# Kernel optimization log

Hardware: AMD Instinct MI355X
Metric: run time of the kernel (lower is better)

The kernel has to match this reference:

```python
import jax, jax.numpy as jnp
import numpy as np

B, TT, C, H, T = 4, 4096, 1024, 16, 128
K = C // H  # head size (rk and v head sizes equal here)
HEAD_DIV = 8.0  # head_size_divisor
EPS = 1e-5  # GroupNorm eps
LAYER_ID, N_LAYER = 12, 24


def setup_inputs() -> dict:
    key = jax.random.key(0)
    ks = jax.random.split(key, 8)
    r01 = LAYER_ID / (N_LAYER - 1)
    r1a0 = 1.0 - LAYER_ID / N_LAYER
    ddd = (jnp.arange(C, dtype=jnp.float32) / C).reshape(1, 1, C)
    h = jnp.arange(H, dtype=jnp.float32)
    scale = 0.02
    return {
        "xq": jax.random.normal(ks[0], (B, TT, C), jnp.float32),
        "time_mix_k": ddd ** r1a0,
        "time_mix_v": ddd ** r1a0 + 0.3 * r01,
        "time_mix_r": ddd ** (0.5 * r1a0),
        "time_mix_g": ddd ** (0.5 * r1a0),
        "time_decay": -8.0 + 7.0 * (h / (H - 1)) ** (0.7 + 1.3 * r01),
        "time_faaaa": r01 * (1.0 - h / (H - 1)),
        "W_r": jax.random.normal(ks[1], (C, C), jnp.float32) * scale,
        "W_k": jax.random.normal(ks[2], (C, C), jnp.float32) * scale,
        "W_v": jax.random.normal(ks[3], (C, C), jnp.float32) * scale,
        "W_g": jax.random.normal(ks[4], (C, C), jnp.float32) * scale,
        "W_o": jax.random.normal(ks[5], (C, C), jnp.float32) * scale,
        "ln_w": jnp.ones((C,), jnp.float32),
        "ln_b": jnp.zeros((C,), jnp.float32),
    }


def reference(xq, time_mix_k, time_mix_v, time_mix_r, time_mix_g,
              time_decay, time_faaaa, W_r, W_k, W_v, W_g, W_o, ln_w, ln_b):
    x = xq
    B_, TT_, C_ = x.shape
    N = TT_ // T  # number of chunks
    # time shift: xx[:, t] = x[:, t-1], xx[:, 0] = 0
    xx = jnp.pad(x, ((0, 0), (1, 0), (0, 0)))[:, :-1]
    xr = x * time_mix_r + xx * (1 - time_mix_r)
    xk = x * time_mix_k + xx * (1 - time_mix_k)
    xv = x * time_mix_v + xx * (1 - time_mix_v)
    xg = x * time_mix_g + xx * (1 - time_mix_g)
    r = (xr @ W_r.T).reshape(B_, TT_, H, K).transpose(0, 2, 1, 3)  # (B,H,TT,K)
    k = (xk @ W_k.T).reshape(B_, TT_, H, K).transpose(0, 2, 1, 3)
    v = (xv @ W_v.T).reshape(B_, TT_, H, K).transpose(0, 2, 1, 3)
    g = jax.nn.silu(xg @ W_g.T)  # (B,TT,C)

    decay = jnp.exp(-jnp.exp(time_decay))  # (H,)
    u = time_faaaa  # (H,)
    ws = decay ** T  # per-chunk state decay (H,)
    i_idx = jnp.arange(T)
    wb = decay[:, None] ** i_idx                # (H,T): decay^i
    wk = decay[:, None] ** (T - 1 - i_idx)      # (H,T): decay^(T-1-j)
    diff = i_idx[:, None] - i_idx[None, :]      # i - j
    pw = decay[:, None, None] ** jnp.maximum(diff - 1, 0)
    # lower-triangular intra-chunk decay: decay^(i-j-1) for i>j, u on diag
    w_mat = jnp.where(diff > 0, pw, 0.0) + jnp.eye(T, dtype=x.dtype) * u[:, None, None]  # (H,T,T)

    # chunked layout: (N, B, H, T, K)
    rc = r.reshape(B_, H, N, T, K).transpose(2, 0, 1, 3, 4)
    kc = k.reshape(B_, H, N, T, K).transpose(2, 0, 1, 3, 4)
    vc = v.reshape(B_, H, N, T, K).transpose(2, 0, 1, 3, 4)
    s0 = jnp.zeros((B_, H, K, K), x.dtype)

    def step(s, chunk):
        rr, kk, vv = chunk
        att = jnp.einsum('bhik,bhjk->bhij', rr, kk) * w_mat
        out = att @ vv + jnp.einsum('bhik,bhkv->bhiv', rr, s) * wb[None, :, :, None]
        s_new = ws[None, :, None, None] * s + jnp.einsum(
            'bhjk,bhjv->bhkv', kk * wk[None, :, :, None], vv)
        return s_new, out

    _, xo = jax.lax.scan(step, s0, (rc, kc, vc))  # xo: (N,B,H,T,K)
    xo = xo.transpose(1, 0, 3, 2, 4).reshape(B_, TT_, H, K)

    # GroupNorm(H groups) over channels, applied to x / head_size_divisor
    y = xo / HEAD_DIV
    mu = y.mean(-1, keepdims=True)
    var = y.var(-1, keepdims=True)
    y = (y - mu) / jnp.sqrt(var + EPS)
    y = y * ln_w.reshape(H, K) + ln_b.reshape(H, K)
    y = y.reshape(B_, TT_, C_)
    return (y * g) @ W_o.T
```

## Files before the change

### kernel.cpp

```cpp
#include <hip/hip_runtime.h>
#include <hip/hip_bf16.h>
#include <stdint.h>

#define C_DIM 1024
#define H_DIM 16
#define K_DIM 64
#define T_CH 128
#define TT_DIM 4096
#define B_DIM 4
#define N_CH 32
#define M_ROWS 16384

typedef __attribute__((ext_vector_type(8))) __bf16 bf16x8;
typedef __attribute__((ext_vector_type(4))) float floatx4;

__device__ __forceinline__ float bf2f(ushort u) {
  union { uint32_t i; float f; } v; v.i = ((uint32_t)u) << 16; return v.f;
}
__device__ __forceinline__ ushort f2bf(float f) {
  union { float f; uint32_t i; } v; v.f = f;
  return (ushort)((v.i + 0x7fffu + ((v.i >> 16) & 1u)) >> 16);
}

#define GLOAD_LDS16(g, l)                                                     \
  __builtin_amdgcn_global_load_lds(                                           \
      (const __attribute__((address_space(1))) void*)(g),                     \
      (__attribute__((address_space(3))) void*)(l), 16, 0, 0)

__global__ __launch_bounds__(256) void mix_kernel(
    const float* __restrict__ x,
    const float* __restrict__ mk, const float* __restrict__ mv,
    const float* __restrict__ mr, const float* __restrict__ mg,
    ushort* __restrict__ xr, ushort* __restrict__ xk,
    ushort* __restrict__ xv, ushort* __restrict__ xg) {
  long idx = (long)blockIdx.x * 256 + threadIdx.x;
  long e = idx * 8;
  int c = (int)(e & (C_DIM - 1));
  long row = e >> 10;
  int t = (int)(row & (TT_DIM - 1));
  floatx4 xc0 = *(const floatx4*)(x + e);
  floatx4 xc1 = *(const floatx4*)(x + e + 4);
  floatx4 xp0 = {0.f, 0.f, 0.f, 0.f};
  floatx4 xp1 = {0.f, 0.f, 0.f, 0.f};
  if (t != 0) {
    xp0 = *(const floatx4*)(x + e - C_DIM);
    xp1 = *(const floatx4*)(x + e - C_DIM + 4);
  }
  floatx4 d0 = xc0 - xp0;
  floatx4 d1 = xc1 - xp1;
  union { ushort u[8]; uint4 q; } pk;
#define ST(dst, mptr)                                                         \
  {                                                                           \
    floatx4 m0 = *(const floatx4*)((mptr) + c);                               \
    floatx4 m1 = *(const floatx4*)((mptr) + c + 4);                           \
    floatx4 o0 = xp0 + d0 * m0;                                               \
    floatx4 o1 = xp1 + d1 * m1;                                               \
    pk.u[0] = f2bf(o0.x); pk.u[1] = f2bf(o0.y);                               \
    pk.u[2] = f2bf(o0.z); pk.u[3] = f2bf(o0.w);                               \
    pk.u[4] = f2bf(o1.x); pk.u[5] = f2bf(o1.y);                               \
    pk.u[6] = f2bf(o1.z); pk.u[7] = f2bf(o1.w);                               \
    *(uint4*)((dst) + e) = pk.q;                                              \
  }
  ST(xk, mk) ST(xv, mv) ST(xr, mr) ST(xg, mg)
#undef ST
}

__global__ __launch_bounds__(256) void wconv_kernel(
    const float* __restrict__ w0, const float* __restrict__ w1,
    const float* __restrict__ w2, const float* __restrict__ w3,
    const float* __restrict__ w4, ushort* __restrict__ o) {
  long idx = (long)blockIdx.x * 256 + threadIdx.x;
  long e = idx * 8;
  int wi = (int)(e >> 20);
  long off = e & ((1L << 20) - 1);
  const float* src = wi == 0 ? w0 : wi == 1 ? w1 : wi == 2 ? w2 : wi == 3 ? w3 : w4;
  floatx4 v0 = *(const floatx4*)(src + off);
  floatx4 v1 = *(const floatx4*)(src + off + 4);
  union { ushort u[8]; uint4 q; } pk;
  pk.u[0] = f2bf(v0.x); pk.u[1] = f2bf(v0.y);
  pk.u[2] = f2bf(v0.z); pk.u[3] = f2bf(v0.w);
  pk.u[4] = f2bf(v1.x); pk.u[5] = f2bf(v1.y);
  pk.u[6] = f2bf(v1.z); pk.u[7] = f2bf(v1.w);
  *(uint4*)(o + e) = pk.q;
}

#define BARX() __builtin_amdgcn_s_barrier()
#define SCHEDB() __builtin_amdgcn_sched_barrier(0)
#define VMW4() asm volatile("s_waitcnt vmcnt(4)" ::: "memory")
#define VMW0() asm volatile("s_waitcnt vmcnt(0)" ::: "memory")
#define LGKW() asm volatile("s_waitcnt lgkmcnt(0)" ::: "memory")

template <int EPI>
__global__ __launch_bounds__(512, 2) void gemm_bt(
    const ushort* __restrict__ A, const ushort* __restrict__ Bt,
    void* __restrict__ Cout) {
  __shared__ __align__(16) ushort smem[65536];
  const int tid = threadIdx.x;
  const int lane = tid & 63, w = tid >> 6;
  const int q = lane >> 4, l16 = lane & 15;
  const int wm = w >> 2, wn = w & 3;
  const int id = blockIdx.x;
  const int wg = (id & 7) * 32 + (id >> 3);
  const int bm = wg >> 2, bn = wg & 3;

  const int r8 = tid >> 3;
  const int c8 = ((tid & 7) ^ (r8 & 7)) * 8;
  const ushort* gA = A + (long)(bm * 256 + r8) * C_DIM + c8;
  const ushort* gB = Bt + (long)(bn * 256 + r8) * C_DIM + c8;

  const char* sB = (const char*)smem;
  const int arow = (wm * 128 + l16) * 128;
  const int brow = (wn * 64 + l16) * 128;
  const int swz = (l16 & 7) << 4;
  const int csv[2] = {(q << 4) ^ swz, ((4 + q) << 4) ^ swz};

  floatx4 acc[8][4] = {};
  bf16x8 af[4][2];
  bf16x8 bfv[4][2];

#define STAGE(ISA, sl, hh, tile)                                              \
  do {                                                                        \
    const ushort* g_ = (ISA ? gA : gB) + ((hh) * 131072 + (tile) * 64);       \
    ushort* l_ = smem + ((ISA ? 0 : 32768) + (sl) * 16384 + (hh) * 8192 +     \
                         w * 512);                                            \
    GLOAD_LDS16(g_, l_);                                                      \
    GLOAD_LDS16(g_ + 65536, l_ + 4096);                                       \
  } while (0)

#define READ_A(sl, qr)                                                        \
  do {                                                                        \
    _Pragma("unroll") for (int i_ = 0; i_ < 4; ++i_) {                        \
      af[i_][0] = *(const bf16x8*)(sB + (sl) * 32768 + arow + (qr) * 8192 +   \
                                   i_ * 2048 + csv[0]);                       \
      af[i_][1] = *(const bf16x8*)(sB + (sl) * 32768 + arow + (qr) * 8192 +   \
                                   i_ * 2048 + csv[1]);                       \
    }                                                                         \
  } while (0)

#define READ_B(sl, qc)                                                        \
  do {                                                                        \
    _Pragma("unroll") for (int j_ = 0; j_ < 2; ++j_) {                        \
      bfv[(qc) * 2 + j_][0] = *(const bf16x8*)(sB + 65536 + (sl) * 32768 +    \
                                               brow + (qc) * 4096 +           \
                                               j_ * 2048 + csv[0]);           \
      bfv[(qc) * 2 + j_][1] = *(const bf16x8*)(sB + 65536 + (sl) * 32768 +    \
                                               brow + (qc) * 4096 +           \
                                               j_ * 2048 + csv[1]);           \
    }                                                                         \
  } while (0)

#define MFMA_Q(qr, qc)                                                        \
  do {                                                                        \
    __builtin_amdgcn_s_setprio(1);                                            \
    _Pragma("unroll") for (int i_ = 0; i_ < 4; ++i_)                          \
        _Pragma("unroll") for (int j_ = 0; j_ < 2; ++j_) {                    \
      acc[(qr) * 4 + i_][(qc) * 2 + j_] =                                     \
          __builtin_amdgcn_mfma_f32_16x16x32_bf16(                            \
              af[i_][0], bfv[(qc) * 2 + j_][0],                               \
              acc[(qr) * 4 + i_][(qc) * 2 + j_], 0, 0, 0);                    \
      acc[(qr) * 4 + i_][(qc) * 2 + j_] =                                     \
          __builtin_amdgcn_mfma_f32_16x16x32_bf16(                            \
              af[i_][1], bfv[(qc) * 2 + j_][1],                               \
              acc[(qr) * 4 + i_][(qc) * 2 + j_], 0, 0, 0);                    \
    }                                                                         \
    __builtin_amdgcn_s_setprio(0);                                            \
  } while (0)

  STAGE(1, 0, 0, 0); STAGE(1, 0, 1, 0);
  STAGE(0, 0, 0, 0); STAGE(0, 0, 1, 0);
  STAGE(0, 1, 0, 1); STAGE(0, 1, 1, 1);
  VMW4();
  BARX();
  SCHEDB();
  READ_B(0, 0);

#pragma unroll 1
  for (int i = 0; i < 7; ++i) {
    const int t1 = 2 * i + 1, tn0 = 2 * i + 2, tn1 = 2 * i + 3;
    READ_A(0, 0); STAGE(1, 1, 0, t1);
    BARX(); SCHEDB(); READ_B(0, 1); MFMA_Q(0, 0); LGKW(); BARX();
    STAGE(1, 1, 1, t1);
    BARX(); SCHEDB(); MFMA_Q(0, 1); LGKW(); BARX();
    READ_A(0, 1); STAGE(0, 0, 0, tn0);
    BARX(); SCHEDB(); MFMA_Q(1, 0); LGKW(); BARX();
    STAGE(0, 0, 1, tn0); VMW4();
    BARX(); SCHEDB(); READ_B(1, 0); MFMA_Q(1, 1); LGKW(); BARX();
    READ_A(1, 0); STAGE(1, 0, 0, tn0);
    BARX(); SCHEDB(); READ_B(1, 1); MFMA_Q(0, 0); LGKW(); BARX();
    STAGE(1, 0, 1, tn0);
    BARX(); SCHEDB(); MFMA_Q(0, 1); LGKW(); BARX();
    READ_A(1, 1); STAGE(0, 1, 0, tn1);
    BARX(); SCHEDB(); MFMA_Q(1, 0); LGKW(); BARX();
    STAGE(0, 1, 1, tn1); VMW4();
    BARX(); SCHEDB(); READ_B(0, 0); MFMA_Q(1, 1); LGKW(); BARX();
  }
  READ_A(0, 0); STAGE(1, 1, 0, 15);
  BARX(); SCHEDB(); READ_B(0, 1); MFMA_Q(0, 0); LGKW(); BARX();
  STAGE(1, 1, 1, 15);
  BARX(); SCHEDB(); MFMA_Q(0, 1); LGKW(); BARX();
  READ_A(0, 1);
  BARX(); SCHEDB(); MFMA_Q(1, 0); LGKW(); BARX();
  VMW0();
  BARX(); SCHEDB(); READ_B(1, 0); MFMA_Q(1, 1); LGKW(); BARX();
  READ_A(1, 0);
  BARX(); SCHEDB(); READ_B(1, 1); MFMA_Q(0, 0); LGKW(); BARX();
  BARX(); SCHEDB(); MFMA_Q(0, 1); LGKW(); BARX();
  READ_A(1, 1);
  BARX(); SCHEDB(); MFMA_Q(1, 0); LGKW(); BARX();
  BARX(); MFMA_Q(1, 1);

  const int row0 = bm * 256 + wm * 128 + q * 4;
  const int col0 = bn * 256 + wn * 64 + l16;
#pragma unroll
  for (int fi = 0; fi < 8; ++fi)
#pragma unroll
    for (int fj = 0; fj < 4; ++fj)
#pragma unroll
      for (int rg = 0; rg < 4; ++rg) {
        long off = (long)(row0 + fi * 16 + rg) * C_DIM + col0 + fj * 16;
        float val = acc[fi][fj][rg];
        if (EPI == 1) val = val / (1.f + expf(-val));
        if (EPI == 2)
          ((float*)Cout)[off] = val;
        else
          ((ushort*)Cout)[off] = f2bf(val);
      }
#undef STAGE
#undef READ_A
#undef READ_B
#undef MFMA_Q
}

__global__ __launch_bounds__(256) void chunk_state(
    const ushort* __restrict__ kB, const ushort* __restrict__ vB,
    const float* __restrict__ td, ushort* __restrict__ Zc) {
  __shared__ __align__(16) ushort vt_s[64 * 136];
  __shared__ __align__(16) ushort kwt_s[64 * 136];
  int blk = blockIdx.x;
  int bh = blk >> 5, n = blk & 31;
  int b = bh >> 4, h = bh & 15;
  int tid = threadIdx.x;
  int lane = tid & 63, w = tid >> 6;
  int q = lane >> 4, l16 = lane & 15;
  float etd = expf(td[h]);
  long cbase = ((long)b * TT_DIM + n * T_CH) * C_DIM + h * K_DIM;

#pragma unroll
  for (int it = 0; it < 4; it++) {
    int chunk = it * 256 + tid;
    int row = chunk >> 3;
    int cc = (chunk & 7) * 8;
    long ga = cbase + (long)row * C_DIM + cc;
    uint4 kv4 = *(const uint4*)(kB + ga);
    uint4 vv4 = *(const uint4*)(vB + ga);
    float wkj = expf(-(float)(T_CH - 1 - row) * etd);
    const ushort* kp = (const ushort*)&kv4;
    const ushort* vp = (const ushort*)&vv4;
    int cb2 = row >> 3;
#pragma unroll
    for (int e2 = 0; e2 < 8; e2++) {
      int vr = cc + e2;
      int ph = vr * 136 + ((cb2 ^ ((vr >> 3) & 7)) << 3) + (row & 7);
      kwt_s[ph] = f2bf(bf2f(kp[e2]) * wkj);
      vt_s[ph] = vp[e2];
    }
  }
  __syncthreads();

  floatx4 accZ[4] = {};
#pragma unroll
  for (int js = 0; js < 128; js += 32) {
    int cb = q + (js >> 3);
    int vrA = w * 16 + l16;
    bf16x8 av = *(const bf16x8*)&vt_s[vrA * 136 + ((cb ^ ((vrA >> 3) & 7)) << 3)];
    bf16x8 bk3[4];
#pragma unroll
    for (int kt = 0; kt < 4; kt++) {
      int vrB = kt * 16 + l16;
      bk3[kt] = *(const bf16x8*)&kwt_s[vrB * 136 + ((cb ^ ((vrB >> 3) & 7)) << 3)];
    }
#pragma unroll
    for (int kt = 0; kt < 4; kt++)
      accZ[kt] = __builtin_amdgcn_mfma_f32_16x16x32_bf16(av, bk3[kt], accZ[kt], 0, 0, 0);
  }
  long zbase = (long)blk * 4096;
#pragma unroll
  for (int kt = 0; kt < 4; kt++)
#pragma unroll
    for (int rg = 0; rg < 4; rg++)
      Zc[zbase + (w * 16 + q * 4 + rg) * 64 + kt * 16 + l16] = f2bf(accZ[kt][rg]);
}

__global__ __launch_bounds__(256) void state_scan(
    const ushort* __restrict__ Zc, const float* __restrict__ td,
    ushort* __restrict__ Sb) {
  long tg = (long)blockIdx.x * 256 + threadIdx.x;
  int bh = (int)(tg >> 12);
  int e = (int)(tg & 4095);
  int h = bh & 15;
  float wsf = expf(-128.f * expf(td[h]));
  float s = 0.f;
  long base = (long)bh * N_CH * 4096 + e;
#pragma unroll
  for (int n = 0; n < N_CH; n++) {
    Sb[base + n * 4096] = f2bf(s);
    s = wsf * s + bf2f(Zc[base + n * 4096]);
  }
}

__global__ __launch_bounds__(512, 4) void chunk_out(
    const ushort* __restrict__ rB, const ushort* __restrict__ kB,
    const ushort* __restrict__ vB, const ushort* __restrict__ gBuf,
    const ushort* __restrict__ Sb,
    const float* __restrict__ td, const float* __restrict__ tf,
    const float* __restrict__ lnw, const float* __restrict__ lnb,
    ushort* __restrict__ gy) {
  __shared__ __align__(16) ushort rr_s[128 * 72];
  __shared__ __align__(16) ushort un_s[128 * 136];
  __shared__ __align__(16) ushort vt_s[64 * 136];
  __shared__ __align__(16) ushort z_s[64 * 72];
  __shared__ float pw_s[128];

  int blk = blockIdx.x;
  int bh = blk >> 5, n = blk & 31;
  int b = bh >> 4, h = bh & 15;
  int tid = threadIdx.x;
  int lane = tid & 63, w = tid >> 6;
  int q = lane >> 4, l16 = lane & 15;

  float etd = expf(td[h]);
  float u = tf[h];
  long cbase = ((long)b * TT_DIM + n * T_CH) * C_DIM + h * K_DIM;

  if (tid < 128) pw_s[tid] = expf(-(float)tid * etd);

#pragma unroll
  for (int it = 0; it < 2; it++) {
    int chunk = it * 512 + tid;
    int row = chunk >> 3;
    int cc = (chunk & 7) * 8;
    long ga = cbase + (long)row * C_DIM + cc;
    *(uint4*)&rr_s[row * 72 + cc] = *(const uint4*)(rB + ga);
    *(uint4*)&un_s[row * 136 + cc] = *(const uint4*)(kB + ga);
    uint4 vv4 = *(const uint4*)(vB + ga);
    const ushort* vp = (const ushort*)&vv4;
    int cb2 = row >> 3;
#pragma unroll
    for (int e2 = 0; e2 < 8; e2++) {
      int vr = cc + e2;
      vt_s[vr * 136 + ((cb2 ^ ((vr >> 3) & 7)) << 3) + (row & 7)] = vp[e2];
    }
  }
  {
    long sbase = (long)blk * 4096;
    int v = tid >> 3, c0 = (tid & 7) * 8;
    *(uint4*)&z_s[v * 72 + c0] = *(const uint4*)(Sb + sbase + v * 64 + c0);
  }
  __syncthreads();

  int ar0 = (w >> 1) * 32, ac0 = (w & 1) * 64;
  floatx4 accA[2][4] = {};
#pragma unroll
  for (int ks = 0; ks < 64; ks += 32) {
    bf16x8 af[2], bk2[4];
#pragma unroll
    for (int i = 0; i < 2; i++)
      af[i] = *(const bf16x8*)&rr_s[(ar0 + i * 16 + l16) * 72 + q * 8 + ks];
#pragma unroll
    for (int j = 0; j < 4; j++)
      bk2[j] = *(const bf16x8*)&un_s[(ac0 + j * 16 + l16) * 136 + q * 8 + ks];
#pragma unroll
    for (int mi = 0; mi < 2; mi++)
#pragma unroll
      for (int nj = 0; nj < 4; nj++)
        accA[mi][nj] = __builtin_amdgcn_mfma_f32_16x16x32_bf16(
            af[mi], bk2[nj], accA[mi][nj], 0, 0, 0);
  }

  int i0 = w * 16;
  floatx4 accB[4] = {};
#pragma unroll
  for (int ks = 0; ks < 64; ks += 32) {
    bf16x8 af2 = *(const bf16x8*)&rr_s[(i0 + l16) * 72 + q * 8 + ks];
    bf16x8 bz[4];
#pragma unroll
    for (int vt2 = 0; vt2 < 4; vt2++)
      bz[vt2] = *(const bf16x8*)&z_s[(vt2 * 16 + l16) * 72 + q * 8 + ks];
#pragma unroll
    for (int vt2 = 0; vt2 < 4; vt2++)
      accB[vt2] = __builtin_amdgcn_mfma_f32_16x16x32_bf16(
          af2, bz[vt2], accB[vt2], 0, 0, 0);
  }
  __syncthreads();

#pragma unroll
  for (int mi = 0; mi < 2; mi++)
#pragma unroll
    for (int nj = 0; nj < 4; nj++)
#pragma unroll
      for (int rg = 0; rg < 4; rg++) {
        int i = ar0 + mi * 16 + q * 4 + rg;
        int j = ac0 + nj * 16 + l16;
        float wv = 0.f;
        if (i > j) wv = pw_s[i - j - 1];
        else if (i == j) wv = u;
        un_s[i * 136 + j] = f2bf(accA[mi][nj][rg] * wv);
      }
  __syncthreads();

  floatx4 accO[4] = {};
#pragma unroll
  for (int js = 0; js < 128; js += 32) {
    bf16x8 af3 = *(const bf16x8*)&un_s[(i0 + l16) * 136 + q * 8 + js];
    int cb = q + (js >> 3);
    bf16x8 bv[4];
#pragma unroll
    for (int vt2 = 0; vt2 < 4; vt2++) {
      int vr = vt2 * 16 + l16;
      bv[vt2] = *(const bf16x8*)&vt_s[vr * 136 + ((cb ^ ((vr >> 3) & 7)) << 3)];
    }
#pragma unroll
    for (int vt2 = 0; vt2 < 4; vt2++)
      accO[vt2] = __builtin_amdgcn_mfma_f32_16x16x32_bf16(
          af3, bv[vt2], accO[vt2], 0, 0, 0);
  }

#pragma unroll
  for (int rg = 0; rg < 4; rg++) {
    int i = i0 + q * 4 + rg;
    float wbi = pw_s[i];
    float vals[4];
    float s1 = 0.f, s2 = 0.f;
#pragma unroll
    for (int vt2 = 0; vt2 < 4; vt2++) {
      float val = accO[vt2][rg] + wbi * accB[vt2][rg];
      vals[vt2] = val; s1 += val; s2 += val * val;
    }
#pragma unroll
    for (int mm = 1; mm < 16; mm <<= 1) {
      s1 += __shfl_xor(s1, mm, 64);
      s2 += __shfl_xor(s2, mm, 64);
    }
    float mu = s1 * (1.f / 64.f);
    float va = s2 * (1.f / 64.f) - mu * mu;
    float rinv = rsqrtf(va + 64.f * 1e-5f);
    long rowg = (long)b * TT_DIM + n * T_CH + i;
#pragma unroll
    for (int vt2 = 0; vt2 < 4; vt2++) {
      int c = h * K_DIM + vt2 * 16 + l16;
      float y = (vals[vt2] - mu) * rinv * lnw[c] + lnb[c];
      float gf = bf2f(gBuf[rowg * C_DIM + c]);
      gy[rowg * C_DIM + c] = f2bf(y * gf);
    }
  }
}

extern "C" void kernel_launch(void* const* d_in, const int* in_sizes, int n_in,
                              void* d_out, int out_size, void* d_ws,
                              size_t ws_size, hipStream_t stream) {
  const float* xq  = (const float*)d_in[0];
  const float* tmk = (const float*)d_in[1];
  const float* tmv = (const float*)d_in[2];
  const float* tmr = (const float*)d_in[3];
  const float* tmg = (const float*)d_in[4];
  const float* td  = (const float*)d_in[5];
  const float* tf  = (const float*)d_in[6];
  const float* Wr  = (const float*)d_in[7];
  const float* Wk  = (const float*)d_in[8];
  const float* Wv  = (const float*)d_in[9];
  const float* Wg  = (const float*)d_in[10];
  const float* Wo  = (const float*)d_in[11];
  const float* lnw = (const float*)d_in[12];
  const float* lnb = (const float*)d_in[13];

  char* ws = (char*)d_ws;
  const size_t BUF = (size_t)M_ROWS * C_DIM * 2;
  ushort* b0 = (ushort*)(ws + 0 * BUF);
  ushort* b1 = (ushort*)(ws + 1 * BUF);
  ushort* b2 = (ushort*)(ws + 2 * BUF);
  ushort* b3 = (ushort*)(ws + 3 * BUF);
  ushort* wcv = (ushort*)(ws + 4 * BUF);
  const ushort* wr_b = wcv;
  const ushort* wk_b = wcv + (1 << 20);
  const ushort* wv_b = wcv + 2 * (1 << 20);
  const ushort* wg_b = wcv + 3 * (1 << 20);
  const ushort* wo_b = wcv + 4 * (1 << 20);
  ushort* Zc = (ushort*)(ws + 4 * BUF + 5 * (2 << 20));
  ushort* Sb = Zc + (size_t)64 * N_CH * 4096;
  ushort* rbuf = (ushort*)d_out;

  mix_kernel<<<8192, 256, 0, stream>>>(xq, tmk, tmv, tmr, tmg, b0, b1, b2, b3);
  wconv_kernel<<<2560, 256, 0, stream>>>(Wr, Wk, Wv, Wg, Wo, wcv);

  gemm_bt<0><<<256, 512, 0, stream>>>(b0, wr_b, rbuf);
  gemm_bt<0><<<256, 512, 0, stream>>>(b1, wk_b, b0);
  gemm_bt<0><<<256, 512, 0, stream>>>(b2, wv_b, b1);
  gemm_bt<1><<<256, 512, 0, stream>>>(b3, wg_b, b2);

  chunk_state<<<2048, 256, 0, stream>>>(b0, b1, td, Zc);
  state_scan<<<1024, 256, 0, stream>>>(Zc, td, Sb);
  chunk_out<<<2048, 512, 0, stream>>>(rbuf, b0, b1, b2, Sb, td, tf, lnw, lnb, b3);

  gemm_bt<2><<<256, 512, 0, stream>>>(b3, wo_b, (float*)d_out);
}
```

Before: 405.8 us.

## Fuse time-shift mixing into projection GEMM A-operand loading

Removes the standalone mix kernel and adds a gemm_mix kernel. It loads fp32 x and the shifted previous row, applies the per-channel mix coefficient, converts to bf16 and writes the A tile into LDS inside the GEMM pipeline. This avoids writing four bf16 mixed activation buffers to memory and reading them back. In exchange each of the four GEMMs reads fp32 x twice (current and previous row), roughly four times the A-operand bytes of before. It also adds VALU conversion work and register pressure inside the MFMA loop.

```diff
diff --git a/kernel.cpp b/kernel.cpp
--- a/kernel.cpp
+++ b/kernel.cpp
@@ -26,44 +26,6 @@
   __builtin_amdgcn_global_load_lds(                                           \
       (const __attribute__((address_space(1))) void*)(g),                     \
       (__attribute__((address_space(3))) void*)(l), 16, 0, 0)
-
-__global__ __launch_bounds__(256) void mix_kernel(
-    const float* __restrict__ x,
-    const float* __restrict__ mk, const float* __restrict__ mv,
-    const float* __restrict__ mr, const float* __restrict__ mg,
-    ushort* __restrict__ xr, ushort* __restrict__ xk,
-    ushort* __restrict__ xv, ushort* __restrict__ xg) {
-  long idx = (long)blockIdx.x * 256 + threadIdx.x;
-  long e = idx * 8;
-  int c = (int)(e & (C_DIM - 1));
-  long row = e >> 10;
-  int t = (int)(row & (TT_DIM - 1));
-  floatx4 xc0 = *(const floatx4*)(x + e);
-  floatx4 xc1 = *(const floatx4*)(x + e + 4);
-  floatx4 xp0 = {0.f, 0.f, 0.f, 0.f};
-  floatx4 xp1 = {0.f, 0.f, 0.f, 0.f};
-  if (t != 0) {
-    xp0 = *(const floatx4*)(x + e - C_DIM);
-    xp1 = *(const floatx4*)(x + e - C_DIM + 4);
-  }
-  floatx4 d0 = xc0 - xp0;
-  floatx4 d1 = xc1 - xp1;
-  union { ushort u[8]; uint4 q; } pk;
-#define ST(dst, mptr)                                                         \
-  {                                                                           \
-    floatx4 m0 = *(const floatx4*)((mptr) + c);                               \
-    floatx4 m1 = *(const floatx4*)((mptr) + c + 4);                           \
-    floatx4 o0 = xp0 + d0 * m0;                                               \
-    floatx4 o1 = xp1 + d1 * m1;                                               \
-    pk.u[0] = f2bf(o0.x); pk.u[1] = f2bf(o0.y);                               \
-    pk.u[2] = f2bf(o0.z); pk.u[3] = f2bf(o0.w);                               \
-    pk.u[4] = f2bf(o1.x); pk.u[5] = f2bf(o1.y);                               \
-    pk.u[6] = f2bf(o1.z); pk.u[7] = f2bf(o1.w);                               \
-    *(uint4*)((dst) + e) = pk.q;                                              \
-  }
-  ST(xk, mk) ST(xv, mv) ST(xr, mr) ST(xg, mg)
-#undef ST
-}
 
 __global__ __launch_bounds__(256) void wconv_kernel(
     const float* __restrict__ w0, const float* __restrict__ w1,
@@ -87,8 +49,200 @@
 #define BARX() __builtin_amdgcn_s_barrier()
 #define SCHEDB() __builtin_amdgcn_sched_barrier(0)
 #define VMW4() asm volatile("s_waitcnt vmcnt(4)" ::: "memory")
+#define VMW22() asm volatile("s_waitcnt vmcnt(22)" ::: "memory")
 #define VMW0() asm volatile("s_waitcnt vmcnt(0)" ::: "memory")
 #define LGKW() asm volatile("s_waitcnt lgkmcnt(0)" ::: "memory")
+
+template <int EPI>
+__global__ __launch_bounds__(512, 2) void gemm_mix(
+    const float* __restrict__ X, const float* __restrict__ coef,
+    const ushort* __restrict__ Bt, void* __restrict__ Cout) {
+  __shared__ __align__(16) ushort smem[65536];
+  const int tid = threadIdx.x;
+  const int lane = tid & 63, w = tid >> 6;
+  const int q = lane >> 4, l16 = lane & 15;
+  const int wm = w >> 2, wn = w & 3;
+  const int id = blockIdx.x;
+  const int wg = (id & 7) * 32 + (id >> 3);
+  const int bm = wg >> 2, bn = wg & 3;
+
+  const int r8 = tid >> 3;
+  const int c8 = ((tid & 7) ^ (r8 & 7)) * 8;
+  const int arowg = bm * 256 + r8;
+  const float* Xb = X + (long)arowg * C_DIM + c8;
+  const float* Cfb = coef + c8;
+  const ushort* gB = Bt + (long)(bn * 256 + r8) * C_DIM + c8;
+
+  const char* sB = (const char*)smem;
+  const int arow = (wm * 128 + l16) * 128;
+  const int brow = (wn * 64 + l16) * 128;
+  const int swz = (l16 & 7) << 4;
+  const int csv[2] = {(q << 4) ^ swz, ((4 + q) << 4) ^ swz};
+
+  floatx4 acc[8][4] = {};
+  bf16x8 af[4][2];
+  bf16x8 bfv[4][2];
+  floatx4 mxc[4], mxp[4], mcf[2];
+
+#define STAGE_B(sl, hh, tile)                                                 \
+  do {                                                                        \
+    const ushort* g_ = gB + ((hh) * 131072 + (tile) * 64);                    \
+    ushort* l_ = smem + (32768 + (sl) * 16384 + (hh) * 8192 + w * 512);       \
+    GLOAD_LDS16(g_, l_);                                                      \
+    GLOAD_LDS16(g_ + 65536, l_ + 4096);                                       \
+  } while (0)
+
+#define MISSUE(tile, hh, WCF)                                                 \
+  do {                                                                        \
+    const float* p0_ = Xb + ((long)((hh) * 128) << 10) + (tile) * 64;         \
+    const float* p1_ = p0_ + (64 << 10);                                      \
+    mxc[0] = *(const floatx4*)p0_;                                            \
+    mxc[1] = *(const floatx4*)(p0_ + 4);                                      \
+    mxc[2] = *(const floatx4*)p1_;                                            \
+    mxc[3] = *(const floatx4*)(p1_ + 4);                                      \
+    floatx4 z_ = {0.f, 0.f, 0.f, 0.f};                                        \
+    if (((arowg + (hh) * 128) & (TT_DIM - 1)) != 0) {                         \
+      mxp[0] = *(const floatx4*)(p0_ - C_DIM);                                \
+      mxp[1] = *(const floatx4*)(p0_ - C_DIM + 4);                            \
+    } else { mxp[0] = z_; mxp[1] = z_; }                                      \
+    if (((arowg + (hh) * 128 + 64) & (TT_DIM - 1)) != 0) {                    \
+      mxp[2] = *(const floatx4*)(p1_ - C_DIM);                                \
+      mxp[3] = *(const floatx4*)(p1_ - C_DIM + 4);                            \
+    } else { mxp[2] = z_; mxp[3] = z_; }                                      \
+    if (WCF) {                                                                \
+      mcf[0] = *(const floatx4*)(Cfb + (tile) * 64);                          \
+      mcf[1] = *(const floatx4*)(Cfb + (tile) * 64 + 4);                      \
+    }                                                                         \
+  } while (0)
+
+#define MWRITE(sl, hh)                                                        \
+  do {                                                                        \
+    union { ushort u[8]; uint4 qq; } pk_;                                     \
+    floatx4 d0_ = mxc[0] - mxp[0];                                            \
+    floatx4 o0_ = mxp[0] + d0_ * mcf[0];                                      \
+    floatx4 d1_ = mxc[1] - mxp[1];                                            \
+    floatx4 o1_ = mxp[1] + d1_ * mcf[1];                                      \
+    pk_.u[0] = f2bf(o0_.x); pk_.u[1] = f2bf(o0_.y);                           \
+    pk_.u[2] = f2bf(o0_.z); pk_.u[3] = f2bf(o0_.w);                           \
+    pk_.u[4] = f2bf(o1_.x); pk_.u[5] = f2bf(o1_.y);                           \
+    pk_.u[6] = f2bf(o1_.z); pk_.u[7] = f2bf(o1_.w);                           \
+    *(uint4*)(smem + ((sl) * 16384 + (hh) * 8192 + tid * 8)) = pk_.qq;        \
+    floatx4 d2_ = mxc[2] - mxp[2];                                            \
+    floatx4 o2_ = mxp[2] + d2_ * mcf[0];                                      \
+    floatx4 d3_ = mxc[3] - mxp[3];                                            \
+    floatx4 o3_ = mxp[3] + d3_ * mcf[1];                                      \
+    pk_.u[0] = f2bf(o2_.x); pk_.u[1] = f2bf(o2_.y);                           \
+    pk_.u[2] = f2bf(o2_.z); pk_.u[3] = f2bf(o2_.w);                           \
+    pk_.u[4] = f2bf(o3_.x); pk_.u[5] = f2bf(o3_.y);                           \
+    pk_.u[6] = f2bf(o3_.z); pk_.u[7] = f2bf(o3_.w);                           \
+    *(uint4*)(smem + ((sl) * 16384 + (hh) * 8192 + 4096 + tid * 8)) = pk_.qq; \
+  } while (0)
+
+#define READ_A(sl, qr)                                                        \
+  do {                                                                        \
+    _Pragma("unroll") for (int i_ = 0; i_ < 4; ++i_) {                        \
+      af[i_][0] = *(const bf16x8*)(sB + (sl) * 32768 + arow + (qr) * 8192 +   \
+                                   i_ * 2048 + csv[0]);                       \
+      af[i_][1] = *(const bf16x8*)(sB + (sl) * 32768 + arow + (qr) * 8192 +   \
+                                   i_ * 2048 + csv[1]);                       \
+    }                                                                         \
+  } while (0)
+
+#define READ_B(sl, qc)                                                        \
+  do {                                                                        \
+    _Pragma("unroll") for (int j_ = 0; j_ < 2; ++j_) {                        \
+      bfv[(qc) * 2 + j_][0] = *(const bf16x8*)(sB + 65536 + (sl) * 32768 +    \
+                                               brow + (qc) * 4096 +           \
+                                               j_ * 2048 + csv[0]);           \
+      bfv[(qc) * 2 + j_][1] = *(const bf16x8*)(sB + 65536 + (sl) * 32768 +    \
+                                               brow + (qc) * 4096 +           \
+                                               j_ * 2048 + csv[1]);           \
+    }                                                                         \
+  } while (0)
+
+#define MFMA_Q(qr, qc)                                                        \
+  do {                                                                        \
+    __builtin_amdgcn_s_setprio(1);                                            \
+    _Pragma("unroll") for (int i_ = 0; i_ < 4; ++i_)                          \
+        _Pragma("unroll") for (int j_ = 0; j_ < 2; ++j_) {                    \
+      acc[(qr) * 4 + i_][(qc) * 2 + j_] =                                     \
+          __builtin_amdgcn_mfma_f32_16x16x32_bf16(                            \
+              af[i_][0], bfv[(qc) * 2 + j_][0],                               \
+              acc[(qr) * 4 + i_][(qc) * 2 + j_], 0, 0, 0);                    \
+      acc[(qr) * 4 + i_][(qc) * 2 + j_] =                                     \
+          __builtin_amdgcn_mfma_f32_16x16x32_bf16(                            \
+              af[i_][1], bfv[(qc) * 2 + j_][1],                               \
+              acc[(qr) * 4 + i_][(qc) * 2 + j_], 0, 0, 0);                    \
+    }                                                                         \
+    __builtin_amdgcn_s_setprio(0);                                            \
+  } while (0)
+
+  MISSUE(0, 0, 1); MWRITE(0, 0);
+  MISSUE(0, 1, 0); MWRITE(0, 1);
+  STAGE_B(0, 0, 0); STAGE_B(0, 1, 0);
+  STAGE_B(1, 0, 1); STAGE_B(1, 1, 1);
+  MISSUE(1, 0, 1);
+  VMW4();
+  LGKW();
+  BARX();
+  SCHEDB();
+  READ_B(0, 0);
+
+#pragma unroll 1
+  for (int i = 0; i < 7; ++i) {
+    const int t1 = 2 * i + 1, tn0 = 2 * i + 2, tn1 = 2 * i + 3;
+    READ_A(0, 0); MWRITE(1, 0); MISSUE(t1, 1, 0);
+    BARX(); SCHEDB(); READ_B(0, 1); MFMA_Q(0, 0); LGKW(); BARX();
+    MWRITE(1, 1);
+    BARX(); SCHEDB(); MFMA_Q(0, 1); LGKW(); BARX();
+    READ_A(0, 1); STAGE_B(0, 0, tn0);
+    BARX(); SCHEDB(); MFMA_Q(1, 0); LGKW(); BARX();
+    STAGE_B(0, 1, tn0); MISSUE(tn0, 0, 1); VMW22();
+    BARX(); SCHEDB(); READ_B(1, 0); MFMA_Q(1, 1); LGKW(); BARX();
+    READ_A(1, 0); MWRITE(0, 0); MISSUE(tn0, 1, 0);
+    BARX(); SCHEDB(); READ_B(1, 1); MFMA_Q(0, 0); LGKW(); BARX();
+    MWRITE(0, 1);
+    BARX(); SCHEDB(); MFMA_Q(0, 1); LGKW(); BARX();
+    READ_A(1, 1); STAGE_B(1, 0, tn1);
+    BARX(); SCHEDB(); MFMA_Q(1, 0); LGKW(); BARX();
+    STAGE_B(1, 1, tn1); MISSUE(tn1, 0, 1); VMW22();
+    BARX(); SCHEDB(); READ_B(0, 0); MFMA_Q(1, 1); LGKW(); BARX();
+  }
+  READ_A(0, 0); MWRITE(1, 0); MISSUE(15, 1, 0);
+  BARX(); SCHEDB(); READ_B(0, 1); MFMA_Q(0, 0); LGKW(); BARX();
+  MWRITE(1, 1);
+  BARX(); SCHEDB(); MFMA_Q(0, 1); LGKW(); BARX();
+  READ_A(0, 1);
+  BARX(); SCHEDB(); MFMA_Q(1, 0); LGKW(); BARX();
+  VMW0();
+  BARX(); SCHEDB(); READ_B(1, 0); MFMA_Q(1, 1); LGKW(); BARX();
+  READ_A(1, 0);
+  BARX(); SCHEDB(); READ_B(1, 1); MFMA_Q(0, 0); LGKW(); BARX();
+  BARX(); SCHEDB(); MFMA_Q(0, 1); LGKW(); BARX();
+  READ_A(1, 1);
+  BARX(); SCHEDB(); MFMA_Q(1, 0); LGKW(); BARX();
+  BARX(); MFMA_Q(1, 1);
+
+  const int row0 = bm * 256 + wm * 128 + q * 4;
+  const int col0 = bn * 256 + wn * 64 + l16;
+#pragma unroll
+  for (int fi = 0; fi < 8; ++fi)
+#pragma unroll
+    for (int fj = 0; fj < 4; ++fj)
+#pragma unroll
+      for (int rg = 0; rg < 4; ++rg) {
+        long off = (long)(row0 + fi * 16 + rg) * C_DIM + col0 + fj * 16;
+        float val = acc[fi][fj][rg];
+        if (EPI == 1) val = val / (1.f + expf(-val));
+        ((ushort*)Cout)[off] = f2bf(val);
+      }
+#undef STAGE_B
+#undef MISSUE
+#undef MWRITE
+#undef READ_A
+#undef READ_B
+#undef MFMA_Q
+}
 
 template <int EPI>
 __global__ __launch_bounds__(512, 2) void gemm_bt(
@@ -489,13 +643,12 @@
   ushort* Sb = Zc + (size_t)64 * N_CH * 4096;
   ushort* rbuf = (ushort*)d_out;
 
-  mix_kernel<<<8192, 256, 0, stream>>>(xq, tmk, tmv, tmr, tmg, b0, b1, b2, b3);
   wconv_kernel<<<2560, 256, 0, stream>>>(Wr, Wk, Wv, Wg, Wo, wcv);
 
-  gemm_bt<0><<<256, 512, 0, stream>>>(b0, wr_b, rbuf);
-  gemm_bt<0><<<256, 512, 0, stream>>>(b1, wk_b, b0);
-  gemm_bt<0><<<256, 512, 0, stream>>>(b2, wv_b, b1);
-  gemm_bt<1><<<256, 512, 0, stream>>>(b3, wg_b, b2);
+  gemm_mix<0><<<256, 512, 0, stream>>>(xq, tmr, wr_b, rbuf);
+  gemm_mix<0><<<256, 512, 0, stream>>>(xq, tmk, wk_b, b0);
+  gemm_mix<0><<<256, 512, 0, stream>>>(xq, tmv, wv_b, b1);
+  gemm_mix<1><<<256, 512, 0, stream>>>(xq, tmg, wg_b, b2);
 
   chunk_state<<<2048, 256, 0, stream>>>(b0, b1, td, Zc);
   state_scan<<<1024, 256, 0, stream>>>(Zc, td, Sb);
```

Measured after the change: 558.5 us. +37.6%, slower.
